# Optimization experiments

Hardware: AMD Instinct MI355X
Metric: run time of the kernel (lower is better)

Reference implementation:

```python
import jax, jax.numpy as jnp
import numpy as np

H, CH = 4, 16          # heads, hidden_features // heads
SLOPE = 0.2            # leaky_relu negative slope


def gat(x, W, a_src, a_dst):
    # x: (B, N, C); W: (hidden, C); a_src/a_dst: (H, CH)
    B, N, _ = x.shape
    h = (x @ W.T).reshape(B, N, H, CH)
    a1 = jnp.einsum('bnhc,hc->bnh', h, a_src)   # att_src scores
    a2 = jnp.einsum('bnhc,hc->bnh', h, a_dst)   # att_dst scores
    # torch: a1.unsqueeze(1) + a2.unsqueeze(2) -> (B, N, N, H)
    e = a1[:, None, :, :] + a2[:, :, None, :]
    e = jnp.transpose(e, (0, 3, 1, 2))          # (B, H, N, N)
    e = jnp.where(e >= 0, e, SLOPE * e)         # leaky_relu
    return jax.nn.softmax(e, axis=2)            # softmax over dim=2 as in torch


def pool(x, W1, b1, W2, b2):
    # diff-pool assignment: (B, N, K), then x' = S^T x -> (B, K, C)
    s = jax.nn.softmax(jax.nn.relu(x @ W1.T + b1) @ W2.T + b2, axis=-1)
    return jnp.einsum('bnk,bnc->bkc', s, x)


def fuse(att0, atts, lefts, rights):
    out = att0
    for a, l, r in zip(atts, lefts, rights):
        # left (H,J0,K) @ att (B,H,K,K) @ right (H,K,J0), broadcast over batch
        out = out + jnp.einsum('hjk,bhkl,hlm->bhjm', l, a, r)
    return out


def setup_inputs() -> dict:
    key = jax.random.key(0)
    ks = iter(jax.random.split(key, 40))
    n = lambda shape, s=0.1: jax.random.normal(next(ks), shape, dtype=jnp.float32) * s
    inp = {
        'src': n((64, 64, 64, 25), 1.0),
        'gat_lin': n((6, 64, 64)), 'gat_asrc': n((6, 4, 16)), 'gat_adst': n((6, 4, 16)),
        'sp0_W1': n((64, 64)), 'sp0_b1': jnp.zeros((64,), jnp.float32),
        'sp0_W2': n((12, 64)), 'sp0_b2': jnp.zeros((12,), jnp.float32),
        'sp1_W1': n((64, 64)), 'sp1_b1': jnp.zeros((64,), jnp.float32),
        'sp1_W2': n((5, 64)), 'sp1_b2': jnp.zeros((5,), jnp.float32),
        'tp0_W1': n((64, 64)), 'tp0_b1': jnp.zeros((64,), jnp.float32),
        'tp0_W2': n((32, 64)), 'tp0_b2': jnp.zeros((32,), jnp.float32),
        'tp1_W1': n((64, 64)), 'tp1_b1': jnp.zeros((64,), jnp.float32),
        'tp1_W2': n((12, 64)), 'tp1_b2': jnp.zeros((12,), jnp.float32),
        'sl0': n((4, 25, 12)), 'sr0': n((4, 12, 25)),
        'sl1': n((4, 25, 5)), 'sr1': n((4, 5, 25)),
        'tl0': n((4, 64, 32)), 'tr0': n((4, 32, 64)),
        'tl1': n((4, 64, 12)), 'tr1': n((4, 12, 64)),
    }
    return inp


def reference(src, gat_lin, gat_asrc, gat_adst,
              sp0_W1, sp0_b1, sp0_W2, sp0_b2, sp1_W1, sp1_b1, sp1_W2, sp1_b2,
              tp0_W1, tp0_b1, tp0_W2, tp0_b2, tp1_W1, tp1_b1, tp1_W2, tp1_b2,
              sl0, sr0, sl1, sr1, tl0, tr0, tl1, tr1):
    B, C, T, J = src.shape
    # ---- spatial branch: attention over joints per (batch, frame) ----
    xs = jnp.transpose(src, (0, 2, 3, 1)).reshape(B * T, J, C)
    a_s0 = gat(xs, gat_lin[0], gat_asrc[0], gat_adst[0])            # (BT,H,25,25)
    xs1 = pool(xs, sp0_W1, sp0_b1, sp0_W2, sp0_b2)                  # (BT,12,C)
    a_s1 = gat(xs1, gat_lin[1], gat_asrc[1], gat_adst[1])           # (BT,H,12,12)
    xs2 = pool(xs1, sp1_W1, sp1_b1, sp1_W2, sp1_b2)                 # (BT,5,C)
    a_s2 = gat(xs2, gat_lin[2], gat_asrc[2], gat_adst[2])           # (BT,H,5,5)
    s_fused = fuse(a_s0, [a_s1, a_s2], [sl0, sl1], [sr0, sr1])
    # ---- temporal branch: attention over frames per (batch, joint) ----
    xt = jnp.transpose(src, (0, 3, 2, 1)).reshape(B * J, T, C)
    a_t0 = gat(xt, gat_lin[3], gat_asrc[3], gat_adst[3])            # (BJ,H,64,64)
    xt1 = pool(xt, tp0_W1, tp0_b1, tp0_W2, tp0_b2)                  # (BJ,32,C)
    a_t1 = gat(xt1, gat_lin[4], gat_asrc[4], gat_adst[4])
    xt2 = pool(xt1, tp1_W1, tp1_b1, tp1_W2, tp1_b2)                 # (BJ,12,C)
    a_t2 = gat(xt2, gat_lin[5], gat_asrc[5], gat_adst[5])
    t_fused = fuse(a_t0, [a_t1, a_t2], [tl0, tl1], [tr0, tr1])
    return (s_fused.reshape(B, T, H, J, J), t_fused.reshape(B, J, H, T, T))
```

## Files before the change

kernel.cpp:

```cpp
#include <hip/hip_runtime.h>

#define DEVINL __device__ __forceinline__

DEVINL float leaky(float v) { return v >= 0.f ? v : 0.2f * v; }

__global__ void wprep_kernel(const float* __restrict__ lin,
                             const float* __restrict__ asrc,
                             const float* __restrict__ adst,
                             float* __restrict__ w_out) {
    int idx = blockIdx.x * blockDim.x + threadIdx.x;
    if (idx >= 6 * 4 * 64) return;
    int c = idx & 63;
    int h = (idx >> 6) & 3;
    int k = idx >> 8;
    const float* L = lin + k * 64 * 64;
    float s1 = 0.f, s2 = 0.f;
    for (int e = 0; e < 16; ++e) {
        float w = L[(h * 16 + e) * 64 + c];
        s1 += w * asrc[(k * 4 + h) * 16 + e];
        s2 += w * adst[(k * 4 + h) * 16 + e];
    }
    w_out[(k * 2 + 0) * 256 + h * 64 + c] = s1;
    w_out[(k * 2 + 1) * 256 + h * 64 + c] = s2;
}

__global__ void wtrans_kernel(const float* __restrict__ s0, const float* __restrict__ s1,
                              const float* __restrict__ t0, const float* __restrict__ t1,
                              const float* __restrict__ s0w2, const float* __restrict__ s1w2,
                              const float* __restrict__ t0w2, const float* __restrict__ t1w2,
                              float* __restrict__ o) {
    int idx = blockIdx.x * 256 + threadIdx.x;
    if (idx < 16384) {
        int m = idx >> 12, r = idx & 4095, c = r >> 6, d = r & 63;
        const float* src = (m == 0) ? s0 : (m == 1) ? s1 : (m == 2) ? t0 : t1;
        o[idx] = src[d * 64 + c];
    } else if (idx < 16384 + 768) {
        int j = idx - 16384, c = j / 12, k = j - 12 * c;
        o[idx] = s0w2[k * 64 + c];
    } else if (idx < 17152 + 512) {
        int j = idx - 17152, c = j >> 3, k = j & 7;
        o[idx] = (k < 5) ? s1w2[k * 64 + c] : 0.f;
    } else if (idx < 17664 + 2048) {
        int j = idx - 17664, c = j >> 5, k = j & 31;
        o[idx] = t0w2[k * 64 + c];
    } else if (idx < 19712 + 768) {
        int j = idx - 19712, c = j / 12, k = j - 12 * c;
        o[idx] = t1w2[k * 64 + c];
    }
}

__global__ void xs_kernel(const float* __restrict__ src, float* __restrict__ xs) {
    int g = blockIdx.x;
    int b = g >> 6, t = g & 63;
    __shared__ float tile[64][26];
    const float* sp = src + b * 102400 + t * 25;
    for (int idx = threadIdx.x; idx < 64 * 25; idx += blockDim.x) {
        int c = idx / 25, j = idx - c * 25;
        tile[c][j] = sp[c * 1600 + j];
    }
    __syncthreads();
    float* op = xs + g * 25 * 64;
    for (int idx = threadIdx.x; idx < 25 * 64; idx += blockDim.x) {
        int j = idx >> 6, c = idx & 63;
        op[idx] = tile[c][j];
    }
}

__global__ void xt_kernel(const float* __restrict__ src, float* __restrict__ xt) {
    int g = blockIdx.x;
    int b = g / 25, j = g - b * 25;
    __shared__ float tile[64][65];
    const float* sp = src + b * 102400 + j;
    for (int idx = threadIdx.x; idx < 64 * 64; idx += blockDim.x) {
        int c = idx >> 6, t = idx & 63;
        tile[c][t] = sp[c * 1600 + t * 25];
    }
    __syncthreads();
    float* op = xt + g * 64 * 64;
    for (int idx = threadIdx.x; idx < 64 * 64; idx += blockDim.x) {
        int t = idx >> 6, c = idx & 63;
        op[idx] = tile[c][t];
    }
}

template <int N>
__global__ __launch_bounds__(256) void gat_kernel(
    const float* __restrict__ x,
    const float* __restrict__ w,
    float* __restrict__ att) {
    int g = blockIdx.x;
    const int tid = threadIdx.x;
    __shared__ float xlT[64][N + 1];
    __shared__ float wl[512];
    __shared__ float a1s[4 * N], a2s[4 * N];
    __shared__ float mxs[4];
    __shared__ float mjs[4 * N], invs[4 * N];
    const float* xp = x + (size_t)g * N * 64;
    for (int idx = tid; idx < N * 64; idx += 256) {
        int n = idx >> 6, c = idx & 63;
        xlT[c][n] = xp[idx];
    }
    for (int idx = tid; idx < 512; idx += 256) wl[idx] = w[idx];
    __syncthreads();
    for (int idx = tid; idx < 8 * N; idx += 256) {
        int n = idx % N;
        int hh = (idx / N) & 3;
        int sd = idx / (4 * N);
        const float* wp = wl + sd * 256 + hh * 64;
        float acc = 0.f;
        #pragma unroll 8
        for (int c = 0; c < 64; ++c) acc += xlT[c][n] * wp[c];
        (sd == 0 ? a1s : a2s)[hh * N + n] = acc;
    }
    __syncthreads();
    if (tid < 4) {
        float m = -1e30f;
        for (int i = 0; i < N; ++i) m = fmaxf(m, a2s[tid * N + i]);
        mxs[tid] = m;
    }
    __syncthreads();
    for (int idx = tid; idx < 4 * N; idx += 256) {
        int hh = idx / N;
        float aj = a1s[idx];
        float mj = leaky(aj + mxs[hh]);
        float ssum = 0.f;
        for (int i = 0; i < N; ++i) ssum += __expf(leaky(aj + a2s[hh * N + i]) - mj);
        mjs[idx] = mj;
        invs[idx] = 1.f / ssum;
    }
    __syncthreads();
    float* ob = att + (size_t)g * 4 * N * N;
    if constexpr ((N % 4) == 0) {
        constexpr int NF4 = N / 4;
        for (int idx = tid; idx < 4 * N * NF4; idx += 256) {
            int row = idx / NF4;
            int j0 = (idx - row * NF4) * 4;
            int hh = row / N, i = row - hh * N;
            float4 q1 = *(const float4*)&a1s[hh * N + j0];
            float4 qm = *(const float4*)&mjs[hh * N + j0];
            float4 qv = *(const float4*)&invs[hh * N + j0];
            float a2i = a2s[hh * N + i];
            float a1v[4] = {q1.x, q1.y, q1.z, q1.w};
            float mv[4] = {qm.x, qm.y, qm.z, qm.w};
            float iv[4] = {qv.x, qv.y, qv.z, qv.w};
            float r[4];
            #pragma unroll
            for (int c = 0; c < 4; ++c) {
                float e = a1v[c] + a2i;
                e = e >= 0.f ? e : 0.2f * e;
                r[c] = __expf(e - mv[c]) * iv[c];
            }
            *(float4*)&ob[row * N + j0] = make_float4(r[0], r[1], r[2], r[3]);
        }
    } else {
        for (int idx = tid; idx < 4 * N * N; idx += 256) {
            int hh = idx / (N * N), rem = idx - hh * N * N;
            int i = rem / N, j = rem - i * N;
            float e = a1s[hh * N + j] + a2s[hh * N + i];
            e = e >= 0.f ? e : 0.2f * e;
            ob[idx] = __expf(e - mjs[hh * N + j]) * invs[hh * N + j];
        }
    }
}

template <int N, int K, int KP>
__global__ __launch_bounds__(256, 3) void pool_kernel(
    const float* __restrict__ x,
    const float* __restrict__ W1T,
    const float* __restrict__ b1,
    const float* __restrict__ W2T,
    const float* __restrict__ b2,
    float* __restrict__ xo) {
    constexpr int NP = (N + 3) & ~3;
    constexpr int LDN = NP + 1;
    __shared__ float xlT[64 * LDN];
    __shared__ float yT[64 * LDN];
    __shared__ float sT[KP * LDN];
    const int g = blockIdx.x, tid = threadIdx.x;
    const float* xp = x + (size_t)g * N * 64;
    for (int i4 = tid; i4 < N * 16; i4 += 256) {
        int n = i4 >> 4, c0 = (i4 & 15) << 2;
        float4 v = ((const float4*)xp)[i4];
        xlT[(c0 + 0) * LDN + n] = v.x;
        xlT[(c0 + 1) * LDN + n] = v.y;
        xlT[(c0 + 2) * LDN + n] = v.z;
        xlT[(c0 + 3) * LDN + n] = v.w;
    }
    if constexpr (NP > N) {
        for (int i = tid; i < 64 * (NP - N); i += 256) {
            int c = i / (NP - N), n = N + i % (NP - N);
            xlT[c * LDN + n] = 0.f;
        }
    }
    __syncthreads();
    constexpr int T1 = (NP / 4) * 16;
    if (tid < T1) {
        int d0 = (tid & 15) << 2, n0 = (tid >> 4) << 2;
        float acc[4][4] = {};
        #pragma unroll 4
        for (int c = 0; c < 64; ++c) {
            float4 w4 = *(const float4*)(W1T + c * 64 + d0);
            float wv[4] = {w4.x, w4.y, w4.z, w4.w};
            float xv[4];
            #pragma unroll
            for (int r = 0; r < 4; ++r) xv[r] = xlT[c * LDN + n0 + r];
            #pragma unroll
            for (int r = 0; r < 4; ++r)
                #pragma unroll
                for (int cc = 0; cc < 4; ++cc) acc[r][cc] += xv[r] * wv[cc];
        }
        float4 b4 = *(const float4*)(b1 + d0);
        float bb[4] = {b4.x, b4.y, b4.z, b4.w};
        #pragma unroll
        for (int r = 0; r < 4; ++r)
            #pragma unroll
            for (int cc = 0; cc < 4; ++cc)
                yT[(d0 + cc) * LDN + n0 + r] = fmaxf(acc[r][cc] + bb[cc], 0.f);
    }
    __syncthreads();
    constexpr int KG4 = KP / 4;
    constexpr int T2 = (NP / 4) * KG4;
    if (tid < T2) {
        int k0 = (tid % KG4) << 2, n0 = (tid / KG4) << 2;
        float acc[4][4] = {};
        #pragma unroll 4
        for (int d = 0; d < 64; ++d) {
            float4 w4 = *(const float4*)(W2T + d * KP + k0);
            float wv[4] = {w4.x, w4.y, w4.z, w4.w};
            float yv[4];
            #pragma unroll
            for (int r = 0; r < 4; ++r) yv[r] = yT[d * LDN + n0 + r];
            #pragma unroll
            for (int r = 0; r < 4; ++r)
                #pragma unroll
                for (int cc = 0; cc < 4; ++cc) acc[r][cc] += yv[r] * wv[cc];
        }
        #pragma unroll
        for (int cc = 0; cc < 4; ++cc) {
            int k = k0 + cc;
            float bb = (k < K) ? b2[k] : 0.f;
            #pragma unroll
            for (int r = 0; r < 4; ++r)
                sT[k * LDN + n0 + r] = (k < K) ? (acc[r][cc] + bb) : -1e30f;
        }
    }
    __syncthreads();
    if (tid < NP) {
        float m = -1e30f;
        #pragma unroll
        for (int k = 0; k < KP; ++k) m = fmaxf(m, sT[k * LDN + tid]);
        float sum = 0.f;
        float e[KP];
        #pragma unroll
        for (int k = 0; k < KP; ++k) { e[k] = __expf(sT[k * LDN + tid] - m); sum += e[k]; }
        float inv = 1.f / sum;
        #pragma unroll
        for (int k = 0; k < KP; ++k) sT[k * LDN + tid] = e[k] * inv;
    }
    __syncthreads();
    constexpr int KG2 = (K + 1) / 2;
    constexpr int T3 = KG2 * 16;
    if (tid < T3) {
        int k0 = (tid % KG2) * 2, c0 = (tid / KG2) * 4;
        float acc0[4] = {}, acc1[4] = {};
        #pragma unroll 4
        for (int n = 0; n < N; ++n) {
            float sv0 = sT[k0 * LDN + n];
            float sv1 = sT[(k0 + 1) * LDN + n];
            float xv[4];
            #pragma unroll
            for (int j = 0; j < 4; ++j) xv[j] = xlT[(c0 + j) * LDN + n];
            #pragma unroll
            for (int j = 0; j < 4; ++j) { acc0[j] += sv0 * xv[j]; acc1[j] += sv1 * xv[j]; }
        }
        float* op = xo + (size_t)g * K * 64;
        *(float4*)&op[k0 * 64 + c0] = make_float4(acc0[0], acc0[1], acc0[2], acc0[3]);
        if (k0 + 1 < K)
            *(float4*)&op[(k0 + 1) * 64 + c0] = make_float4(acc1[0], acc1[1], acc1[2], acc1[3]);
    }
}

__global__ __launch_bounds__(256, 5) void gatfuse_t(
    const float* __restrict__ x,
    const float* __restrict__ w,
    const float* __restrict__ A1g,
    const float* __restrict__ L1,
    const float* __restrict__ R1,
    const float* __restrict__ A2g,
    const float* __restrict__ L2,
    const float* __restrict__ R2,
    float* __restrict__ out)
{
    const int bid = blockIdx.x;
    const int g = (bid & 7) | ((bid >> 5) << 3);
    const int h = (bid >> 3) & 3;
    const int tid = threadIdx.x;
    __shared__ float t1T[32 * 64];
    __shared__ float r1l[32 * 64];
    __shared__ float t2T[12 * 64];
    __shared__ float r2l[12 * 64];
    __shared__ float A1T[32 * 32];
    __shared__ float A2T[12 * 13];
    __shared__ float a1s[64], a2s[64], mjs[64], invs[64];

    if (tid < 128) {
        int t = tid & 63, sd = tid >> 6;
        const float4* xr = (const float4*)(x + (size_t)g * 4096 + t * 64);
        const float* wv = w + sd * 256 + h * 64;
        float acc = 0.f;
        #pragma unroll
        for (int q = 0; q < 16; ++q) {
            float4 xv = xr[q];
            acc += xv.x * wv[q * 4] + xv.y * wv[q * 4 + 1] +
                   xv.z * wv[q * 4 + 2] + xv.w * wv[q * 4 + 3];
        }
        (sd == 0 ? a1s : a2s)[t] = acc;
    } else {
        int u = tid - 128;
        const float* a1p = A1g + (size_t)(g * 4 + h) * 1024;
        #pragma unroll
        for (int q = 0; q < 8; ++q) {
            int idx = q * 128 + u;
            A1T[(idx & 31) * 32 + (idx >> 5)] = a1p[idx];
        }
        const float* a2p = A2g + (size_t)(g * 4 + h) * 144;
        for (int idx = u; idx < 144; idx += 128) {
            int k = idx / 12, l = idx - k * 12;
            A2T[l * 13 + k] = a2p[idx];
        }
        const float4* r1p = (const float4*)(R1 + h * 2048);
        #pragma unroll
        for (int q = 0; q < 4; ++q) ((float4*)r1l)[q * 128 + u] = r1p[q * 128 + u];
        const float4* r2p = (const float4*)(R2 + h * 768);
        for (int idx = u; idx < 192; idx += 128) ((float4*)r2l)[idx] = r2p[idx];
    }
    __syncthreads();

    if (tid < 64) {
        float mx = a2s[0];
        for (int i = 1; i < 64; ++i) mx = fmaxf(mx, a2s[i]);
        float aj = a1s[tid];
        float mj = leaky(aj + mx);
        float ssum = 0.f;
        for (int i = 0; i < 64; ++i) ssum += __expf(leaky(aj + a2s[i]) - mj);
        mjs[tid] = mj;
        invs[tid] = 1.f / ssum;
    }
    {
        int j = tid & 63, l0 = (tid >> 6) * 8;
        float lj[32];
        const float4* lp = (const float4*)(L1 + (h * 64 + j) * 32);
        #pragma unroll
        for (int q = 0; q < 8; ++q) {
            float4 v = lp[q];
            lj[q * 4] = v.x; lj[q * 4 + 1] = v.y; lj[q * 4 + 2] = v.z; lj[q * 4 + 3] = v.w;
        }
        for (int l = l0; l < l0 + 8; ++l) {
            const float* ar = &A1T[l * 32];
            float acc = 0.f;
            #pragma unroll
            for (int k = 0; k < 32; ++k) acc += lj[k] * ar[k];
            t1T[l * 64 + j] = acc;
        }
    }
    {
        int j = tid & 63, lb = (tid >> 6) * 3;
        float lj2[12];
        const float* lp2 = L2 + (h * 64 + j) * 12;
        #pragma unroll
        for (int k = 0; k < 12; ++k) lj2[k] = lp2[k];
        for (int l = lb; l < lb + 3; ++l) {
            const float* ar = &A2T[l * 13];
            float acc = 0.f;
            #pragma unroll
            for (int k = 0; k < 12; ++k) acc += lj2[k] * ar[k];
            t2T[l * 64 + j] = acc;
        }
    }
    __syncthreads();

    const int i0 = (tid >> 4) << 2, m0 = (tid & 15) << 2;
    float acc[4][4];
    {
        float4 q1 = *(const float4*)&a1s[m0];
        float4 qm = *(const float4*)&mjs[m0];
        float4 qv = *(const float4*)&invs[m0];
        float4 q2 = *(const float4*)&a2s[i0];
        float am[4] = {q1.x, q1.y, q1.z, q1.w};
        float mv[4] = {qm.x, qm.y, qm.z, qm.w};
        float iv[4] = {qv.x, qv.y, qv.z, qv.w};
        float ai[4] = {q2.x, q2.y, q2.z, q2.w};
        #pragma unroll
        for (int r = 0; r < 4; ++r)
            #pragma unroll
            for (int c = 0; c < 4; ++c) {
                float e = am[c] + ai[r];
                e = e >= 0.f ? e : 0.2f * e;
                acc[r][c] = __expf(e - mv[c]) * iv[c];
            }
    }
    #pragma unroll 8
    for (int l = 0; l < 32; ++l) {
        float4 t4 = *(const float4*)&t1T[l * 64 + i0];
        float4 r4 = *(const float4*)&r1l[l * 64 + m0];
        float tv[4] = {t4.x, t4.y, t4.z, t4.w};
        float rv[4] = {r4.x, r4.y, r4.z, r4.w};
        #pragma unroll
        for (int r = 0; r < 4; ++r)
            #pragma unroll
            for (int c = 0; c < 4; ++c) acc[r][c] += tv[r] * rv[c];
    }
    #pragma unroll 4
    for (int l = 0; l < 12; ++l) {
        float4 t4 = *(const float4*)&t2T[l * 64 + i0];
        float4 r4 = *(const float4*)&r2l[l * 64 + m0];
        float tv[4] = {t4.x, t4.y, t4.z, t4.w};
        float rv[4] = {r4.x, r4.y, r4.z, r4.w};
        #pragma unroll
        for (int r = 0; r < 4; ++r)
            #pragma unroll
            for (int c = 0; c < 4; ++c) acc[r][c] += tv[r] * rv[c];
    }
    float* op = out + (size_t)(g * 4 + h) * 4096;
    #pragma unroll
    for (int r = 0; r < 4; ++r)
        *(float4*)&op[(i0 + r) * 64 + m0] =
            make_float4(acc[r][0], acc[r][1], acc[r][2], acc[r][3]);
}

__global__ __launch_bounds__(256) void gatfuse_s(
    const float* __restrict__ x,
    const float* __restrict__ w,
    const float* __restrict__ A1g,
    const float* __restrict__ L1,
    const float* __restrict__ R1,
    const float* __restrict__ A2g,
    const float* __restrict__ L2,
    const float* __restrict__ R2,
    float* __restrict__ out)
{
    const int g = blockIdx.x;
    const int tid = threadIdx.x;
    const int h = tid >> 6, t = tid & 63;
    __shared__ float xl[25 * 68];
    __shared__ float A1T[4][12 * 12];
    __shared__ float A2T[4][5 * 5];
    __shared__ float t1l[4][25 * 12];
    __shared__ float t2l[4][25 * 5];
    __shared__ float r1l[4][12 * 25];
    __shared__ float r2l[4][5 * 25];
    __shared__ float a1s[4][25], a2s[4][25], mjs[4][32], invs[4][32];

    const float* xp = x + (size_t)g * 1600;
    for (int idx = tid; idx < 1600; idx += 256) {
        int n = idx >> 6, c = idx & 63;
        xl[n * 68 + c] = xp[idx];
    }
    const float* a1p = A1g + (size_t)(g * 4 + h) * 144;
    for (int idx = t; idx < 144; idx += 64) {
        int k = idx / 12, l = idx - k * 12;
        A1T[h][l * 12 + k] = a1p[idx];
    }
    const float* a2p = A2g + (size_t)(g * 4 + h) * 25;
    if (t < 25) {
        int k = t / 5, l = t - 5 * k;
        A2T[h][l * 5 + k] = a2p[t];
    }
    for (int idx = t; idx < 300; idx += 64) r1l[h][idx] = R1[h * 300 + idx];
    for (int idx = t; idx < 125; idx += 64) r2l[h][idx] = R2[h * 125 + idx];
    __syncthreads();

    if (t < 25) {
        const float* ws_ = w + h * 64;
        const float* wd_ = w + 256 + h * 64;
        const float* xr = &xl[t * 68];
        float s1 = 0.f, s2 = 0.f;
        #pragma unroll
        for (int c = 0; c < 64; c += 4) {
            float4 xv = *(const float4*)&xr[c];
            s1 += xv.x * ws_[c] + xv.y * ws_[c + 1] + xv.z * ws_[c + 2] + xv.w * ws_[c + 3];
            s2 += xv.x * wd_[c] + xv.y * wd_[c + 1] + xv.z * wd_[c + 2] + xv.w * wd_[c + 3];
        }
        a1s[h][t] = s1;
        a2s[h][t] = s2;
    }
    __syncthreads();

    if (t < 25) {
        float mx = a2s[h][0];
        for (int i = 1; i < 25; ++i) mx = fmaxf(mx, a2s[h][i]);
        float aj = a1s[h][t];
        float mj = leaky(aj + mx);
        float ssum = 0.f;
        for (int i = 0; i < 25; ++i) ssum += __expf(leaky(aj + a2s[h][i]) - mj);
        mjs[h][t] = mj;
        invs[h][t] = 1.f / ssum;
        float lj[12];
        const float* lp = L1 + (h * 25 + t) * 12;
        #pragma unroll
        for (int k = 0; k < 12; ++k) lj[k] = lp[k];
        #pragma unroll
        for (int l = 0; l < 12; ++l) {
            const float* ar = &A1T[h][l * 12];
            float acc = 0.f;
            #pragma unroll
            for (int k = 0; k < 12; ++k) acc += lj[k] * ar[k];
            t1l[h][t * 12 + l] = acc;
        }
        float lj2[5];
        const float* lp2 = L2 + (h * 25 + t) * 5;
        #pragma unroll
        for (int k = 0; k < 5; ++k) lj2[k] = lp2[k];
        #pragma unroll
        for (int l = 0; l < 5; ++l) {
            const float* ar = &A2T[h][l * 5];
            float acc = 0.f;
            #pragma unroll
            for (int k = 0; k < 5; ++k) acc += lj2[k] * ar[k];
            t2l[h][t * 5 + l] = acc;
        }
    }
    __syncthreads();

    float* op = out + (size_t)(g * 4 + h) * 625;
    for (int idx = t; idx < 625; idx += 64) {
        int i = idx / 25, m = idx - i * 25;
        float e = a1s[h][m] + a2s[h][i];
        e = e >= 0.f ? e : 0.2f * e;
        float val = __expf(e - mjs[h][m]) * invs[h][m];
        const float* t1r = &t1l[h][i * 12];
        const float* r1c = &r1l[h][m];
        #pragma unroll
        for (int l = 0; l < 12; ++l) val += t1r[l] * r1c[l * 25];
        const float* t2r = &t2l[h][i * 5];
        const float* r2c = &r2l[h][m];
        #pragma unroll
        for (int l = 0; l < 5; ++l) val += t2r[l] * r2c[l * 25];
        op[idx] = val;
    }
}

extern "C" void kernel_launch(void* const* d_in, const int* in_sizes, int n_in,
                              void* d_out, int out_size, void* d_ws, size_t ws_size,
                              hipStream_t stream) {
    const float* src    = (const float*)d_in[0];
    const float* lin    = (const float*)d_in[1];
    const float* asrc   = (const float*)d_in[2];
    const float* adst   = (const float*)d_in[3];
    const float* sp0_W1 = (const float*)d_in[4];
    const float* sp0_b1 = (const float*)d_in[5];
    const float* sp0_W2 = (const float*)d_in[6];
    const float* sp0_b2 = (const float*)d_in[7];
    const float* sp1_W1 = (const float*)d_in[8];
    const float* sp1_b1 = (const float*)d_in[9];
    const float* sp1_W2 = (const float*)d_in[10];
    const float* sp1_b2 = (const float*)d_in[11];
    const float* tp0_W1 = (const float*)d_in[12];
    const float* tp0_b1 = (const float*)d_in[13];
    const float* tp0_W2 = (const float*)d_in[14];
    const float* tp0_b2 = (const float*)d_in[15];
    const float* tp1_W1 = (const float*)d_in[16];
    const float* tp1_b1 = (const float*)d_in[17];
    const float* tp1_W2 = (const float*)d_in[18];
    const float* tp1_b2 = (const float*)d_in[19];
    const float* sl0    = (const float*)d_in[20];
    const float* sr0    = (const float*)d_in[21];
    const float* sl1    = (const float*)d_in[22];
    const float* sr1    = (const float*)d_in[23];
    const float* tl0    = (const float*)d_in[24];
    const float* tr0    = (const float*)d_in[25];
    const float* tl1    = (const float*)d_in[26];
    const float* tr1    = (const float*)d_in[27];

    float* out_s = (float*)d_out;
    float* out_t = out_s + 10240000;

    float* ws     = (float*)d_ws;
    float* wbuf   = ws;
    float* wT     = ws + 4096;
    float* region = ws + 24576;

    float* sp0_W1T = wT;
    float* sp1_W1T = wT + 4096;
    float* tp0_W1T = wT + 8192;
    float* tp1_W1T = wT + 12288;
    float* sp0_W2T = wT + 16384;
    float* sp1_W2T = wT + 17152;
    float* tp0_W2T = wT + 17664;
    float* tp1_W2T = wT + 19712;

    float* xs  = region;
    float* xs1 = xs + 6553600;
    float* xs2 = xs1 + 3145728;
    float* as1 = xs2 + 1310720;
    float* as2 = as1 + 2359296;
    float* xt  = region;
    float* xt1 = xt + 6553600;
    float* xt2 = xt1 + 3276800;
    float* at1 = xt2 + 1228800;
    float* at2 = at1 + 6553600;

    wprep_kernel<<<6, 256, 0, stream>>>(lin, asrc, adst, wbuf);
    wtrans_kernel<<<80, 256, 0, stream>>>(sp0_W1, sp1_W1, tp0_W1, tp1_W1,
                                          sp0_W2, sp1_W2, tp0_W2, tp1_W2, wT);

    xs_kernel<<<4096, 256, 0, stream>>>(src, xs);
    pool_kernel<25, 12, 12><<<4096, 256, 0, stream>>>(xs, sp0_W1T, sp0_b1, sp0_W2T, sp0_b2, xs1);
    gat_kernel<12><<<4096, 256, 0, stream>>>(xs1, wbuf + 1 * 512, as1);
    pool_kernel<12, 5, 8><<<4096, 256, 0, stream>>>(xs1, sp1_W1T, sp1_b1, sp1_W2T, sp1_b2, xs2);
    gat_kernel<5><<<4096, 256, 0, stream>>>(xs2, wbuf + 2 * 512, as2);
    gatfuse_s<<<4096, 256, 0, stream>>>(xs, wbuf + 0 * 512, as1, sl0, sr0, as2, sl1, sr1, out_s);

    xt_kernel<<<1600, 256, 0, stream>>>(src, xt);
    pool_kernel<64, 32, 32><<<1600, 256, 0, stream>>>(xt, tp0_W1T, tp0_b1, tp0_W2T, tp0_b2, xt1);
    gat_kernel<32><<<1600, 256, 0, stream>>>(xt1, wbuf + 4 * 512, at1);
    pool_kernel<32, 12, 12><<<1600, 256, 0, stream>>>(xt1, tp1_W1T, tp1_b1, tp1_W2T, tp1_b2, xt2);
    gat_kernel<12><<<1600, 256, 0, stream>>>(xt2, wbuf + 5 * 512, at2);
    gatfuse_t<<<6400, 256, 0, stream>>>(xt, wbuf + 3 * 512, at1, tl0, tr0, at2, tl1, tr1, out_t);
}
```

Baseline: 360.2 us.

## Factor GAT softmax exponentials into row/column terms and restructure fused kernels

Rewrites the leaky-relu softmax as separable products: exp terms per row (rE/rF) and per column (cE/cF) are precomputed, so each output element becomes a select and a multiply instead of an exp. In gatfuse_t the R1/R2 shared-memory staging is dropped in favour of direct global loads, warps are split between the softmax and the L1·A1 products, and launch bounds are raised to 8. gatfuse_s gets padded, transposed R and t layouts so the inner products can use float4 loads. The factored exponentials could lose precision for large score ranges, and the extra phases add synchronisation barriers.

```diff
diff --git a/kernel.cpp b/kernel.cpp
--- a/kernel.cpp
+++ b/kernel.cpp
@@ -93,8 +93,8 @@
     __shared__ float xlT[64][N + 1];
     __shared__ float wl[512];
     __shared__ float a1s[4 * N], a2s[4 * N];
+    __shared__ float rE[4 * N], rF[4 * N], cE[4 * N], cF[4 * N];
     __shared__ float mxs[4];
-    __shared__ float mjs[4 * N], invs[4 * N];
     const float* xp = x + (size_t)g * N * 64;
     for (int idx = tid; idx < N * 64; idx += 256) {
         int n = idx >> 6, c = idx & 63;
@@ -121,12 +121,26 @@
     __syncthreads();
     for (int idx = tid; idx < 4 * N; idx += 256) {
         int hh = idx / N;
-        float aj = a1s[idx];
-        float mj = leaky(aj + mxs[hh]);
-        float ssum = 0.f;
-        for (int i = 0; i < N; ++i) ssum += __expf(leaky(aj + a2s[hh * N + i]) - mj);
-        mjs[idx] = mj;
-        invs[idx] = 1.f / ssum;
+        float d = a2s[idx] - mxs[hh];
+        rE[idx] = __expf(d);
+        rF[idx] = __expf(0.2f * d);
+    }
+    __syncthreads();
+    for (int idx = tid; idx < 4 * N; idx += 256) {
+        int hh = idx / N;
+        float a = a1s[idx], mx = mxs[hh];
+        float mj = leaky(a + mx);
+        float E = __expf(a + mx - mj);
+        float F = __expf(0.2f * (a + mx) - mj);
+        float S1 = 0.f, S2 = 0.f;
+        for (int i = 0; i < N; ++i) {
+            bool c = (a + a2s[hh * N + i] >= 0.f);
+            S1 += c ? rE[hh * N + i] : 0.f;
+            S2 += c ? 0.f : rF[hh * N + i];
+        }
+        float iv = 1.f / (E * S1 + F * S2);
+        cE[idx] = E * iv;
+        cF[idx] = F * iv;
     }
     __syncthreads();
     float* ob = att + (size_t)g * 4 * N * N;
@@ -135,30 +149,28 @@
         for (int idx = tid; idx < 4 * N * NF4; idx += 256) {
             int row = idx / NF4;
             int j0 = (idx - row * NF4) * 4;
-            int hh = row / N, i = row - hh * N;
-            float4 q1 = *(const float4*)&a1s[hh * N + j0];
-            float4 qm = *(const float4*)&mjs[hh * N + j0];
-            float4 qv = *(const float4*)&invs[hh * N + j0];
-            float a2i = a2s[hh * N + i];
+            int hh = row / N;
+            float4 q1 = *(const float4*)&a1s[(row / N) * N + j0];
+            float4 qE = *(const float4*)&cE[hh * N + j0];
+            float4 qF = *(const float4*)&cF[hh * N + j0];
+            float a2i = a2s[row];
+            float rEi = rE[row], rFi = rF[row];
             float a1v[4] = {q1.x, q1.y, q1.z, q1.w};
-            float mv[4] = {qm.x, qm.y, qm.z, qm.w};
-            float iv[4] = {qv.x, qv.y, qv.z, qv.w};
+            float ev[4] = {qE.x, qE.y, qE.z, qE.w};
+            float fv[4] = {qF.x, qF.y, qF.z, qF.w};
             float r[4];
             #pragma unroll
-            for (int c = 0; c < 4; ++c) {
-                float e = a1v[c] + a2i;
-                e = e >= 0.f ? e : 0.2f * e;
-                r[c] = __expf(e - mv[c]) * iv[c];
-            }
+            for (int c = 0; c < 4; ++c)
+                r[c] = (a1v[c] + a2i >= 0.f) ? ev[c] * rEi : fv[c] * rFi;
             *(float4*)&ob[row * N + j0] = make_float4(r[0], r[1], r[2], r[3]);
         }
     } else {
         for (int idx = tid; idx < 4 * N * N; idx += 256) {
             int hh = idx / (N * N), rem = idx - hh * N * N;
             int i = rem / N, j = rem - i * N;
-            float e = a1s[hh * N + j] + a2s[hh * N + i];
-            e = e >= 0.f ? e : 0.2f * e;
-            ob[idx] = __expf(e - mjs[hh * N + j]) * invs[hh * N + j];
+            bool cnd = (a1s[hh * N + j] + a2s[hh * N + i] >= 0.f);
+            ob[idx] = cnd ? cE[hh * N + j] * rE[hh * N + i]
+                          : cF[hh * N + j] * rF[hh * N + i];
         }
     }
 }
@@ -280,7 +292,7 @@
     }
 }
 
-__global__ __launch_bounds__(256, 5) void gatfuse_t(
+__global__ __launch_bounds__(256, 8) void gatfuse_t(
     const float* __restrict__ x,
     const float* __restrict__ w,
     const float* __restrict__ A1g,
@@ -296,12 +308,11 @@
     const int h = (bid >> 3) & 3;
     const int tid = threadIdx.x;
     __shared__ float t1T[32 * 64];
-    __shared__ float r1l[32 * 64];
     __shared__ float t2T[12 * 64];
-    __shared__ float r2l[12 * 64];
-    __shared__ float A1T[32 * 32];
-    __shared__ float A2T[12 * 13];
-    __shared__ float a1s[64], a2s[64], mjs[64], invs[64];
+    __shared__ float A1[32 * 36];
+    __shared__ float A2[12 * 13];
+    __shared__ float a01[64], a02[64];
+    __shared__ float rEs[64], rFs[64], cEs[64], cFs[64];
 
     if (tid < 128) {
         int t = tid & 63, sd = tid >> 6;
@@ -311,69 +322,109 @@
         #pragma unroll
         for (int q = 0; q < 16; ++q) {
             float4 xv = xr[q];
-            acc += xv.x * wv[q * 4] + xv.y * wv[q * 4 + 1] +
-                   xv.z * wv[q * 4 + 2] + xv.w * wv[q * 4 + 3];
-        }
-        (sd == 0 ? a1s : a2s)[t] = acc;
+            float4 w4 = *(const float4*)(wv + q * 4);
+            acc += xv.x * w4.x + xv.y * w4.y + xv.z * w4.z + xv.w * w4.w;
+        }
+        (sd == 0 ? a01 : a02)[t] = acc;
     } else {
         int u = tid - 128;
         const float* a1p = A1g + (size_t)(g * 4 + h) * 1024;
         #pragma unroll
         for (int q = 0; q < 8; ++q) {
             int idx = q * 128 + u;
-            A1T[(idx & 31) * 32 + (idx >> 5)] = a1p[idx];
+            A1[(idx >> 5) * 36 + (idx & 31)] = a1p[idx];
         }
         const float* a2p = A2g + (size_t)(g * 4 + h) * 144;
         for (int idx = u; idx < 144; idx += 128) {
             int k = idx / 12, l = idx - k * 12;
-            A2T[l * 13 + k] = a2p[idx];
-        }
-        const float4* r1p = (const float4*)(R1 + h * 2048);
-        #pragma unroll
-        for (int q = 0; q < 4; ++q) ((float4*)r1l)[q * 128 + u] = r1p[q * 128 + u];
-        const float4* r2p = (const float4*)(R2 + h * 768);
-        for (int idx = u; idx < 192; idx += 128) ((float4*)r2l)[idx] = r2p[idx];
+            A2[k * 13 + l] = a2p[idx];
+        }
     }
     __syncthreads();
 
     if (tid < 64) {
-        float mx = a2s[0];
-        for (int i = 1; i < 64; ++i) mx = fmaxf(mx, a2s[i]);
-        float aj = a1s[tid];
-        float mj = leaky(aj + mx);
-        float ssum = 0.f;
-        for (int i = 0; i < 64; ++i) ssum += __expf(leaky(aj + a2s[i]) - mj);
-        mjs[tid] = mj;
-        invs[tid] = 1.f / ssum;
-    }
-    {
-        int j = tid & 63, l0 = (tid >> 6) * 8;
+        float mx = a02[0];
+        for (int i = 1; i < 64; ++i) mx = fmaxf(mx, a02[i]);
+        float d = a02[tid] - mx;
+        rEs[tid] = __expf(d);
+        rFs[tid] = __expf(0.2f * d);
+        cEs[tid] = mx;
+    } else {
+        const int j = tid & 63, l0 = (tid >> 6) * 8;
         float lj[32];
-        const float4* lp = (const float4*)(L1 + (h * 64 + j) * 32);
+        const float4* lp = (const float4*)(L1 + ((size_t)h * 64 + j) * 32);
         #pragma unroll
         for (int q = 0; q < 8; ++q) {
             float4 v = lp[q];
             lj[q * 4] = v.x; lj[q * 4 + 1] = v.y; lj[q * 4 + 2] = v.z; lj[q * 4 + 3] = v.w;
         }
-        for (int l = l0; l < l0 + 8; ++l) {
-            const float* ar = &A1T[l * 32];
+        float acc8[8] = {};
+        for (int k = 0; k < 32; ++k) {
+            float lk = lj[k];
+            float4 a4a = *(const float4*)&A1[k * 36 + l0];
+            float4 a4b = *(const float4*)&A1[k * 36 + l0 + 4];
+            acc8[0] += lk * a4a.x; acc8[1] += lk * a4a.y;
+            acc8[2] += lk * a4a.z; acc8[3] += lk * a4a.w;
+            acc8[4] += lk * a4b.x; acc8[5] += lk * a4b.y;
+            acc8[6] += lk * a4b.z; acc8[7] += lk * a4b.w;
+        }
+        #pragma unroll
+        for (int lo = 0; lo < 8; ++lo) t1T[(l0 + lo) * 64 + j] = acc8[lo];
+    }
+    __syncthreads();
+
+    if (tid < 64) {
+        float mx = cEs[tid];
+        float a = a01[tid];
+        float mj = leaky(a + mx);
+        float E = __expf(a + mx - mj);
+        float F = __expf(0.2f * (a + mx) - mj);
+        float S1 = 0.f, S2 = 0.f;
+        for (int i = 0; i < 64; ++i) {
+            bool c = (a + a02[i] >= 0.f);
+            S1 += c ? rEs[i] : 0.f;
+            S2 += c ? 0.f : rFs[i];
+        }
+        float iv = 1.f / (E * S1 + F * S2);
+        cEs[tid] = E * iv;
+        cFs[tid] = F * iv;
+    } else if (tid < 128) {
+        const int j = tid & 63;
+        float lj[32];
+        const float4* lp = (const float4*)(L1 + ((size_t)h * 64 + j) * 32);
+        #pragma unroll
+        for (int q = 0; q < 8; ++q) {
+            float4 v = lp[q];
+            lj[q * 4] = v.x; lj[q * 4 + 1] = v.y; lj[q * 4 + 2] = v.z; lj[q * 4 + 3] = v.w;
+        }
+        float acc8[8] = {};
+        for (int k = 0; k < 32; ++k) {
+            float lk = lj[k];
+            float4 a4a = *(const float4*)&A1[k * 36];
+            float4 a4b = *(const float4*)&A1[k * 36 + 4];
+            acc8[0] += lk * a4a.x; acc8[1] += lk * a4a.y;
+            acc8[2] += lk * a4a.z; acc8[3] += lk * a4a.w;
+            acc8[4] += lk * a4b.x; acc8[5] += lk * a4b.y;
+            acc8[6] += lk * a4b.z; acc8[7] += lk * a4b.w;
+        }
+        #pragma unroll
+        for (int lo = 0; lo < 8; ++lo) t1T[lo * 64 + j] = acc8[lo];
+    } else {
+        const int j = tid & 63, lb = ((tid >> 6) - 2) * 6;
+        float lj2[12];
+        const float4* lp2 = (const float4*)(L2 + ((size_t)h * 64 + j) * 12);
+        #pragma unroll
+        for (int q = 0; q < 3; ++q) {
+            float4 v = lp2[q];
+            lj2[q * 4] = v.x; lj2[q * 4 + 1] = v.y;
+            lj2[q * 4 + 2] = v.z; lj2[q * 4 + 3] = v.w;
+        }
+        #pragma unroll
+        for (int lo = 0; lo < 6; ++lo) {
+            int l = lb + lo;
             float acc = 0.f;
             #pragma unroll
-            for (int k = 0; k < 32; ++k) acc += lj[k] * ar[k];
-            t1T[l * 64 + j] = acc;
-        }
-    }
-    {
-        int j = tid & 63, lb = (tid >> 6) * 3;
-        float lj2[12];
-        const float* lp2 = L2 + (h * 64 + j) * 12;
-        #pragma unroll
-        for (int k = 0; k < 12; ++k) lj2[k] = lp2[k];
-        for (int l = lb; l < lb + 3; ++l) {
-            const float* ar = &A2T[l * 13];
-            float acc = 0.f;
-            #pragma unroll
-            for (int k = 0; k < 12; ++k) acc += lj2[k] * ar[k];
+            for (int k = 0; k < 12; ++k) acc += lj2[k] * A2[k * 13 + l];
             t2T[l * 64 + j] = acc;
         }
     }
@@ -382,27 +433,30 @@
     const int i0 = (tid >> 4) << 2, m0 = (tid & 15) << 2;
     float acc[4][4];
     {
-        float4 q1 = *(const float4*)&a1s[m0];
-        float4 qm = *(const float4*)&mjs[m0];
-        float4 qv = *(const float4*)&invs[m0];
-        float4 q2 = *(const float4*)&a2s[i0];
-        float am[4] = {q1.x, q1.y, q1.z, q1.w};
-        float mv[4] = {qm.x, qm.y, qm.z, qm.w};
-        float iv[4] = {qv.x, qv.y, qv.z, qv.w};
-        float ai[4] = {q2.x, q2.y, q2.z, q2.w};
+        float4 qa1 = *(const float4*)&a01[m0];
+        float4 qcE = *(const float4*)&cEs[m0];
+        float4 qcF = *(const float4*)&cFs[m0];
+        float4 qa2 = *(const float4*)&a02[i0];
+        float4 qrE = *(const float4*)&rEs[i0];
+        float4 qrF = *(const float4*)&rFs[i0];
+        float a1v[4] = {qa1.x, qa1.y, qa1.z, qa1.w};
+        float ev[4] = {qcE.x, qcE.y, qcE.z, qcE.w};
+        float fv[4] = {qcF.x, qcF.y, qcF.z, qcF.w};
+        float a2v[4] = {qa2.x, qa2.y, qa2.z, qa2.w};
+        float rev[4] = {qrE.x, qrE.y, qrE.z, qrE.w};
+        float rfv[4] = {qrF.x, qrF.y, qrF.z, qrF.w};
         #pragma unroll
         for (int r = 0; r < 4; ++r)
             #pragma unroll
-            for (int c = 0; c < 4; ++c) {
-                float e = am[c] + ai[r];
-                e = e >= 0.f ? e : 0.2f * e;
-                acc[r][c] = __expf(e - mv[c]) * iv[c];
-            }
-    }
+            for (int c = 0; c < 4; ++c)
+                acc[r][c] = (a1v[c] + a2v[r] >= 0.f) ? ev[c] * rev[r]
+                                                     : fv[c] * rfv[r];
+    }
+    const float* r1b = R1 + (size_t)h * 2048;
     #pragma unroll 8
     for (int l = 0; l < 32; ++l) {
         float4 t4 = *(const float4*)&t1T[l * 64 + i0];
-        float4 r4 = *(const float4*)&r1l[l * 64 + m0];
+        float4 r4 = *(const float4*)(r1b + l * 64 + m0);
         float tv[4] = {t4.x, t4.y, t4.z, t4.w};
         float rv[4] = {r4.x, r4.y, r4.z, r4.w};
         #pragma unroll
@@ -410,10 +464,11 @@
             #pragma unroll
             for (int c = 0; c < 4; ++c) acc[r][c] += tv[r] * rv[c];
     }
+    const float* r2b = R2 + (size_t)h * 768;
     #pragma unroll 4
     for (int l = 0; l < 12; ++l) {
         float4 t4 = *(const float4*)&t2T[l * 64 + i0];
-        float4 r4 = *(const float4*)&r2l[l * 64 + m0];
+        float4 r4 = *(const float4*)(r2b + l * 64 + m0);
         float tv[4] = {t4.x, t4.y, t4.z, t4.w};
         float rv[4] = {r4.x, r4.y, r4.z, r4.w};
         #pragma unroll
@@ -421,14 +476,14 @@
             #pragma unroll
             for (int c = 0; c < 4; ++c) acc[r][c] += tv[r] * rv[c];
     }
-    float* op = out + (size_t)(g * 4 + h) * 4096;
+    float* op = out + ((size_t)g * 4 + h) * 4096;
     #pragma unroll
     for (int r = 0; r < 4; ++r)
         *(float4*)&op[(i0 + r) * 64 + m0] =
             make_float4(acc[r][0], acc[r][1], acc[r][2], acc[r][3]);
 }
 
-__global__ __launch_bounds__(256) void gatfuse_s(
+__global__ __launch_bounds__(256, 5) void gatfuse_s(
     const float* __restrict__ x,
     const float* __restrict__ w,
     const float* __restrict__ A1g,
@@ -443,31 +498,39 @@
     const int tid = threadIdx.x;
     const int h = tid >> 6, t = tid & 63;
     __shared__ float xl[25 * 68];
-    __shared__ float A1T[4][12 * 12];
-    __shared__ float A2T[4][5 * 5];
-    __shared__ float t1l[4][25 * 12];
-    __shared__ float t2l[4][25 * 5];
-    __shared__ float r1l[4][12 * 25];
-    __shared__ float r2l[4][5 * 25];
-    __shared__ float a1s[4][25], a2s[4][25], mjs[4][32], invs[4][32];
+    __shared__ float A1[4][12 * 13];
+    __shared__ float A2[4][5 * 6];
+    __shared__ float t1l[4][25 * 16];
+    __shared__ float t2l[4][25 * 8];
+    __shared__ float r1T[4][25 * 16];
+    __shared__ float r2T[4][25 * 8];
+    __shared__ float a01[4][25], a02[4][25];
+    __shared__ float rE[4][25], rF[4][25], cE[4][25], cF[4][25];
+    __shared__ float mxs[4];
 
     const float* xp = x + (size_t)g * 1600;
-    for (int idx = tid; idx < 1600; idx += 256) {
-        int n = idx >> 6, c = idx & 63;
-        xl[n * 68 + c] = xp[idx];
+    for (int idx = tid; idx < 400; idx += 256) {
+        int n = idx >> 4, c0 = (idx & 15) << 2;
+        *(float4*)&xl[n * 68 + c0] = *(const float4*)(xp + n * 64 + c0);
     }
     const float* a1p = A1g + (size_t)(g * 4 + h) * 144;
     for (int idx = t; idx < 144; idx += 64) {
         int k = idx / 12, l = idx - k * 12;
-        A1T[h][l * 12 + k] = a1p[idx];
+        A1[h][k * 13 + l] = a1p[idx];
     }
     const float* a2p = A2g + (size_t)(g * 4 + h) * 25;
     if (t < 25) {
-        int k = t / 5, l = t - 5 * k;
-        A2T[h][l * 5 + k] = a2p[t];
-    }
-    for (int idx = t; idx < 300; idx += 64) r1l[h][idx] = R1[h * 300 + idx];
-    for (int idx = t; idx < 125; idx += 64) r2l[h][idx] = R2[h * 125 + idx];
+        int k = t / 5, l = t - (t / 5) * 5;
+        A2[h][k * 6 + l] = a2p[t];
+    }
+    for (int idx = t; idx < 400; idx += 64) {
+        int m = idx >> 4, l = idx & 15;
+        r1T[h][idx] = (l < 12) ? R1[h * 300 + l * 25 + m] : 0.f;
+    }
+    for (int idx = t; idx < 200; idx += 64) {
+        int m = idx >> 3, l = idx & 7;
+        r2T[h][idx] = (l < 5) ? R2[h * 125 + l * 25 + m] : 0.f;
+    }
     __syncthreads();
 
     if (t < 25) {
@@ -478,64 +541,95 @@
         #pragma unroll
         for (int c = 0; c < 64; c += 4) {
             float4 xv = *(const float4*)&xr[c];
-            s1 += xv.x * ws_[c] + xv.y * ws_[c + 1] + xv.z * ws_[c + 2] + xv.w * ws_[c + 3];
-            s2 += xv.x * wd_[c] + xv.y * wd_[c + 1] + xv.z * wd_[c + 2] + xv.w * wd_[c + 3];
-        }
-        a1s[h][t] = s1;
-        a2s[h][t] = s2;
+            float4 w1 = *(const float4*)(ws_ + c);
+            float4 w2 = *(const float4*)(wd_ + c);
+            s1 += xv.x * w1.x + xv.y * w1.y + xv.z * w1.z + xv.w * w1.w;
+            s2 += xv.x * w2.x + xv.y * w2.y + xv.z * w2.z + xv.w * w2.w;
+        }
+        a01[h][t] = s1;
+        a02[h][t] = s2;
     }
     __syncthreads();
 
     if (t < 25) {
-        float mx = a2s[h][0];
-        for (int i = 1; i < 25; ++i) mx = fmaxf(mx, a2s[h][i]);
-        float aj = a1s[h][t];
-        float mj = leaky(aj + mx);
-        float ssum = 0.f;
-        for (int i = 0; i < 25; ++i) ssum += __expf(leaky(aj + a2s[h][i]) - mj);
-        mjs[h][t] = mj;
-        invs[h][t] = 1.f / ssum;
+        float mx = a02[h][0];
+        for (int i = 1; i < 25; ++i) mx = fmaxf(mx, a02[h][i]);
+        if (t == 0) mxs[h] = mx;
+        float d = a02[h][t] - mx;
+        rE[h][t] = __expf(d);
+        rF[h][t] = __expf(0.2f * d);
+    } else if (t >= 32 && t < 57) {
+        int i = t - 32;
         float lj[12];
-        const float* lp = L1 + (h * 25 + t) * 12;
-        #pragma unroll
-        for (int k = 0; k < 12; ++k) lj[k] = lp[k];
+        const float4* lp = (const float4*)(L1 + ((size_t)h * 25 + i) * 12);
+        #pragma unroll
+        for (int q = 0; q < 3; ++q) {
+            float4 v = lp[q];
+            lj[q * 4] = v.x; lj[q * 4 + 1] = v.y; lj[q * 4 + 2] = v.z; lj[q * 4 + 3] = v.w;
+        }
         #pragma unroll
         for (int l = 0; l < 12; ++l) {
-            const float* ar = &A1T[h][l * 12];
             float acc = 0.f;
             #pragma unroll
-            for (int k = 0; k < 12; ++k) acc += lj[k] * ar[k];
-            t1l[h][t * 12 + l] = acc;
-        }
+            for (int k = 0; k < 12; ++k) acc += lj[k] * A1[h][k * 13 + l];
+            t1l[h][i * 16 + l] = acc;
+        }
+        #pragma unroll
+        for (int l = 12; l < 16; ++l) t1l[h][i * 16 + l] = 0.f;
         float lj2[5];
-        const float* lp2 = L2 + (h * 25 + t) * 5;
+        const float* lp2 = L2 + ((size_t)h * 25 + i) * 5;
         #pragma unroll
         for (int k = 0; k < 5; ++k) lj2[k] = lp2[k];
         #pragma unroll
         for (int l = 0; l < 5; ++l) {
-            const float* ar = &A2T[h][l * 5];
             float acc = 0.f;
             #pragma unroll
-            for (int k = 0; k < 5; ++k) acc += lj2[k] * ar[k];
-            t2l[h][t * 5 + l] = acc;
-        }
-    }
-    __syncthreads();
-
-    float* op = out + (size_t)(g * 4 + h) * 625;
+            for (int k = 0; k < 5; ++k) acc += lj2[k] * A2[h][k * 6 + l];
+            t2l[h][i * 8 + l] = acc;
+        }
+        #pragma unroll
+        for (int l = 5; l < 8; ++l) t2l[h][i * 8 + l] = 0.f;
+    }
+    __syncthreads();
+
+    if (t < 25) {
+        float a = a01[h][t], mx = mxs[h];
+        float mj = leaky(a + mx);
+        float E = __expf(a + mx - mj);
+        float F = __expf(0.2f * (a + mx) - mj);
+        float S1 = 0.f, S2 = 0.f;
+        for (int i = 0; i < 25; ++i) {
+            bool c = (a + a02[h][i] >= 0.f);
+            S1 += c ? rE[h][i] : 0.f;
+            S2 += c ? 0.f : rF[h][i];
+        }
+        float iv = 1.f / (E * S1 + F * S2);
+        cE[h][t] = E * iv;
+        cF[h][t] = F * iv;
+    }
+    __syncthreads();
+
+    float* op = out + ((size_t)g * 4 + h) * 625;
     for (int idx = t; idx < 625; idx += 64) {
         int i = idx / 25, m = idx - i * 25;
-        float e = a1s[h][m] + a2s[h][i];
-        e = e >= 0.f ? e : 0.2f * e;
-        float val = __expf(e - mjs[h][m]) * invs[h][m];
-        const float* t1r = &t1l[h][i * 12];
-        const float* r1c = &r1l[h][m];
-        #pragma unroll
-        for (int l = 0; l < 12; ++l) val += t1r[l] * r1c[l * 25];
-        const float* t2r = &t2l[h][i * 5];
-        const float* r2c = &r2l[h][m];
-        #pragma unroll
-        for (int l = 0; l < 5; ++l) val += t2r[l] * r2c[l * 25];
+        bool cnd = (a01[h][m] + a02[h][i] >= 0.f);
+        float val = cnd ? cE[h][m] * rE[h][i] : cF[h][m] * rF[h][i];
+        const float* t1r = &t1l[h][i * 16];
+        const float* r1c = &r1T[h][m * 16];
+        #pragma unroll
+        for (int q = 0; q < 4; ++q) {
+            float4 tv = *(const float4*)&t1r[q * 4];
+            float4 rv = *(const float4*)&r1c[q * 4];
+            val += tv.x * rv.x + tv.y * rv.y + tv.z * rv.z + tv.w * rv.w;
+        }
+        const float* t2r = &t2l[h][i * 8];
+        const float* r2c = &r2T[h][m * 8];
+        #pragma unroll
+        for (int q = 0; q < 2; ++q) {
+            float4 tv = *(const float4*)&t2r[q * 4];
+            float4 rv = *(const float4*)&r2c[q * 4];
+            val += tv.x * rv.x + tv.y * rv.y + tv.z * rv.z + tv.w * rv.w;
+        }
         op[idx] = val;
     }
 }
@@ -575,9 +669,9 @@
     float* out_s = (float*)d_out;
     float* out_t = out_s + 10240000;
 
-    float* ws     = (float*)d_ws;
-    float* wbuf   = ws;
-    float* wT     = ws + 4096;
+    float* ws   = (float*)d_ws;
+    float* wbuf = ws;
+    float* wT   = ws + 4096;
     float* region = ws + 24576;
 
     float* sp0_W1T = wT;
```

Result: slower. 419.2 us (+16.4%).
